# Kernel tuning notes

Measured on AMD Instinct MI355X. Metric: run time of the kernel, lower is better.

## Reference

```python
import jax, jax.numpy as jnp
import numpy as np

H = 16
D_MODEL = 1024
D_K = D_MODEL // H
MAX_REL = 16
REL_VOCAB = 2 * MAX_REL + 1


def _rel_pos_ids(seq_len):
    r = jnp.arange(seq_len)
    dist = r[None, :] - r[:, None]                      # [S,S]
    return jnp.clip(dist, -MAX_REL, MAX_REL) + MAX_REL  # in [0, 2*MAX_REL]


def setup_inputs() -> dict:
    key = jax.random.key(0)
    ks = jax.random.split(key, 16)
    B, S = 2, 2048
    f32 = jnp.float32
    inp = {
        "query": jax.random.normal(ks[0], (B, S, D_MODEL), f32),
        "key": jax.random.normal(ks[1], (B, S, D_MODEL), f32),
        "value": jax.random.normal(ks[2], (B, S, D_MODEL), f32),
        # four nn.Linear(d_model, d_model): W [out,in], b [out]
        "Wq": jax.random.normal(ks[3], (D_MODEL, D_MODEL), f32) * 0.02,
        "bq": jnp.zeros((D_MODEL,), f32),
        "Wk": jax.random.normal(ks[4], (D_MODEL, D_MODEL), f32) * 0.02,
        "bk": jnp.zeros((D_MODEL,), f32),
        "Wv": jax.random.normal(ks[5], (D_MODEL, D_MODEL), f32) * 0.02,
        "bv": jnp.zeros((D_MODEL,), f32),
        "Wo": jax.random.normal(ks[6], (D_MODEL, D_MODEL), f32) * 0.02,
        "bo": jnp.zeros((D_MODEL,), f32),
        # relative-position embedding tables (keys and values)
        "rel_k_table": jax.random.normal(ks[7], (REL_VOCAB, D_K), f32) * 0.02,
        "rel_v_table": jax.random.normal(ks[8], (REL_VOCAB, D_K), f32) * 0.02,
    }
    return inp


def reference(query, key, value, Wq, bq, Wk, bk, Wv, bv, Wo, bo,
              rel_k_table, rel_v_table):
    B, S, E = query.shape
    ids = _rel_pos_ids(S)                    # [S,S] int
    rel_k = rel_k_table[ids]                 # [S,S,d_k]
    rel_v = rel_v_table[ids]                 # [S,S,d_k]

    def proj(x, W, b):
        y = x @ W.T + b                      # [B,S,E]
        return y.reshape(B, S, H, D_K).transpose(0, 2, 1, 3)  # [B,H,S,d_k]

    q = proj(query, Wq, bq)
    k = proj(key, Wk, bk)
    v = proj(value, Wv, bv)

    # NOTE: original has no 1/sqrt(d_k) scaling and ignores mask — faithful.
    logits = jnp.einsum('bhqd,bhkd->bhqk', q, k) \
           + jnp.einsum('bhqd,qkd->bhqk', q, rel_k)
    w = jax.nn.softmax(logits, axis=-1)      # [B,H,S,S]

    x = jnp.einsum('bhqk,bhkd->bhqd', w, v) \
      + jnp.einsum('bhqk,qkd->bhqd', w, rel_v)

    x = x.transpose(0, 2, 1, 3).reshape(B, S, H * D_K)
    return x @ Wo.T + bo
```

## Files before the change

kernel.cpp:

```cpp
#include <hip/hip_runtime.h>
#include <hip/hip_bf16.h>

typedef unsigned short u16;
typedef __attribute__((ext_vector_type(8))) short short8;
typedef __attribute__((ext_vector_type(4))) short short4_t;
typedef __attribute__((ext_vector_type(4))) float f32x4;

#define MFMA16(a, b, c) __builtin_amdgcn_mfma_f32_16x16x32_bf16((a), (b), (c), 0, 0, 0)

#if __has_builtin(__builtin_amdgcn_mfma_f32_16x16x16bf16_1k)
#define MFMAK16(a, b, c) __builtin_amdgcn_mfma_f32_16x16x16bf16_1k((a), (b), (c), 0, 0, 0)
#elif __has_builtin(__builtin_amdgcn_mfma_f32_16x16x16_bf16)
#define MFMAK16(a, b, c) __builtin_amdgcn_mfma_f32_16x16x16_bf16((a), (b), (c), 0, 0, 0)
#else
__device__ __forceinline__ f32x4 mfmak16_asm(short4_t a, short4_t b, f32x4 c) {
  asm("v_mfma_f32_16x16x16_bf16 %0, %1, %2, %0" : "+v"(c) : "v"(a), "v"(b));
  return c;
}
#define MFMAK16(a, b, c) mfmak16_asm((a), (b), (c))
#endif

#define GLOAD_LDS16(gp, lp)                                          \
  __builtin_amdgcn_global_load_lds(                                  \
      (const __attribute__((address_space(1))) void*)(gp),           \
      (__attribute__((address_space(3))) void*)(lp), 16, 0, 0)
#define SBAR() asm volatile("s_barrier" ::: "memory")
#define WAIT_LGKM0() asm volatile("s_waitcnt lgkmcnt(0)" ::: "memory")
#define WAIT_VM0() asm volatile("s_waitcnt vmcnt(0)" ::: "memory")

#define LOG2E 1.44269504088896340736f

__device__ __forceinline__ float us2f(u16 u) {
  union { unsigned int i; float f; } c; c.i = ((unsigned int)u) << 16; return c.f;
}
__device__ __forceinline__ u16 f2us(float f) {
  union { float f; unsigned int i; } c; c.f = f;
  return (u16)((c.i + 0x7fffu + ((c.i >> 16) & 1u)) >> 16);
}
__device__ __forceinline__ unsigned int f2us2(float a, float b) {
  union { __hip_bfloat162 h; unsigned int u; } c;
  c.h = __float22bfloat162_rn(float2{a, b});
  return c.u;
}
__device__ __forceinline__ float exp2fast(float x) {
#if __has_builtin(__builtin_amdgcn_exp2f)
  return __builtin_amdgcn_exp2f(x);
#else
  return exp2f(x);
#endif
}

__global__ __launch_bounds__(256) void cvt_all_kernel(
    const float* x0, const float* x1, const float* x2, const float* w0,
    const float* w1, const float* w2, const float* w3, const float* relk,
    u16* y0, u16* y1, u16* y2, u16* z0, u16* z1, u16* z2, u16* z3,
    u16* relkb) {
  const int z = blockIdx.z;
  if (z == 7) {
    const int i = (blockIdx.x * 256 + threadIdx.x) * 8;
    if (i < 4096) {
      if (i < 2112) {
        const float4 a = *(const float4*)(relk + i);
        const float4 b = *(const float4*)(relk + i + 4);
        unsigned int o[4];
        o[0] = f2us2(a.x, a.y); o[1] = f2us2(a.z, a.w);
        o[2] = f2us2(b.x, b.y); o[3] = f2us2(b.z, b.w);
        *(uint4*)(relkb + i) = *(uint4*)o;
      } else {
        uint4 zz = {0u, 0u, 0u, 0u};
        *(uint4*)(relkb + i) = zz;
      }
    }
    return;
  }
  const float* src; u16* dst; int n;
  switch (z) {
    case 0: src = x0; dst = y0; n = 4194304; break;
    case 1: src = x1; dst = y1; n = 4194304; break;
    case 2: src = x2; dst = y2; n = 4194304; break;
    case 3: src = w0; dst = z0; n = 1048576; break;
    case 4: src = w1; dst = z1; n = 1048576; break;
    case 5: src = w2; dst = z2; n = 1048576; break;
    default: src = w3; dst = z3; n = 1048576; break;
  }
  const int i = (blockIdx.x * 256 + threadIdx.x) * 8;
  if (i < n) {
    const float4 a = *(const float4*)(src + i);
    const float4 b = *(const float4*)(src + i + 4);
    unsigned int o[4];
    o[0] = f2us2(a.x, a.y); o[1] = f2us2(a.z, a.w);
    o[2] = f2us2(b.x, b.y); o[3] = f2us2(b.z, b.w);
    *(uint4*)(dst + i) = *(uint4*)o;
  }
}

template <int MODE, typename OUT, int BM, int BN, int BK>
__device__ __forceinline__ void gemm_body(u16* __restrict__ SM,
                                          const u16* __restrict__ X,
                                          const u16* __restrict__ W,
                                          const float* __restrict__ bias,
                                          OUT* __restrict__ Y, int row0, int col0,
                                          float oscale) {
  constexpr int TM = BM / 32, TN = BN / 32;
  constexpr int CH = BK / 8;
  constexpr int RPG = 64 / CH;
  constexpr int NGA = BM / (4 * RPG);
  constexpr int NGB = BN / (4 * RPG);
  u16* As = SM;
  u16* Bs = SM + BM * BK;
  const int tid = threadIdx.x;
  const int lane = tid & 63;
  const int wid = tid >> 6;
  const int wm = wid >> 1, wn = wid & 1;
  const int l15 = lane & 15, l16 = lane >> 4;
  const int lrow = lane / CH;
  const int lch = lane % CH;

  f32x4 acc[TM][TN];
#pragma unroll
  for (int i = 0; i < TM; i++)
#pragma unroll
    for (int j = 0; j < TN; j++) acc[i][j] = (f32x4){0.f, 0.f, 0.f, 0.f};

  for (int k0 = 0; k0 < 1024; k0 += BK) {
#pragma unroll
    for (int i = 0; i < NGA; i++) {
      const int rb = (wid * NGA + i) * RPG;
      const int row = rb + lrow;
      GLOAD_LDS16(X + (size_t)(row0 + row) * 1024 + k0 + ((lch ^ (row & 7)) * 8),
                  &As[rb * BK]);
    }
#pragma unroll
    for (int i = 0; i < NGB; i++) {
      const int rb = (wid * NGB + i) * RPG;
      const int row = rb + lrow;
      GLOAD_LDS16(W + (size_t)(col0 + row) * 1024 + k0 + ((lch ^ (row & 7)) * 8),
                  &Bs[rb * BK]);
    }
    __syncthreads();
#pragma unroll
    for (int kk = 0; kk < BK / 32; kk++) {
      const int ch = kk * 4 + l16;
      short8 af[TM], bfr[TN];
#pragma unroll
      for (int t = 0; t < TM; t++) {
        const int m = wm * (BM / 2) + t * 16 + l15;
        af[t] = *(const short8*)&As[m * BK + ((ch ^ (m & 7)) * 8)];
      }
#pragma unroll
      for (int t = 0; t < TN; t++) {
        const int n = wn * (BN / 2) + t * 16 + l15;
        bfr[t] = *(const short8*)&Bs[n * BK + ((ch ^ (n & 7)) * 8)];
      }
#pragma unroll
      for (int tm = 0; tm < TM; tm++)
#pragma unroll
        for (int tn = 0; tn < TN; tn++)
          acc[tm][tn] = MFMA16(af[tm], bfr[tn], acc[tm][tn]);
    }
    __syncthreads();
  }

  if (MODE == 0) {
#pragma unroll
    for (int tn = 0; tn < TN; tn++) {
      const int col = col0 + wn * (BN / 2) + tn * 16 + l15;
      const float bv = bias[col];
#pragma unroll
      for (int tm = 0; tm < TM; tm++) {
        const int rowb = row0 + wm * (BM / 2) + tm * 16 + l16 * 4;
#pragma unroll
        for (int r = 0; r < 4; r++)
          Y[(size_t)(rowb + r) * 1024 + col] = (OUT)(acc[tm][tn][r] + bv);
      }
    }
  } else {
    u16* T = SM;
    const int bb = row0 >> 11;
    const int sbase = row0 & 2047;
#pragma unroll
    for (int pass = 0; pass < 2; pass++) {
      __syncthreads();
      if (wm == pass) {
#pragma unroll
        for (int tn = 0; tn < TN; tn++) {
          const int coll = wn * 64 + tn * 16 + l15;
          const float bv = bias[col0 + coll];
#pragma unroll
          for (int tm = 0; tm < TM; tm++) {
            if (MODE == 1) {
#pragma unroll
              for (int r = 0; r < 4; r++)
                T[(tm * 16 + l16 * 4 + r) * 136 + coll] = f2us((acc[tm][tn][r] + bv) * oscale);
            } else {
              unsigned int o[2];
              o[0] = f2us2(acc[tm][tn][0] + bv, acc[tm][tn][1] + bv);
              o[1] = f2us2(acc[tm][tn][2] + bv, acc[tm][tn][3] + bv);
              *(short4_t*)&T[coll * 72 + tm * 16 + l16 * 4] = *(short4_t*)o;
            }
          }
        }
      }
      __syncthreads();
      if (MODE == 1) {
#pragma unroll
        for (int i = 0; i < 8; i++) {
          const int idx = tid + i * 256;
          const int srow = idx >> 5, c4 = idx & 31;
          const short4_t v = *(const short4_t*)&T[srow * 136 + c4 * 4];
          const int col = col0 + c4 * 4;
          const int hh = col >> 6, dd = col & 63;
          const int s = sbase + pass * 64 + srow;
          *(short4_t*)&((u16*)Y)[(((size_t)(bb * 16 + hh)) * 2048 + s) * 64 + dd] = v;
        }
      } else {
#pragma unroll
        for (int i = 0; i < 4; i++) {
          const int idx = tid + i * 256;
          const int cl = idx >> 3, sc = idx & 7;
          const short8 v = *(const short8*)&T[cl * 72 + sc * 8];
          const int col = col0 + cl;
          const int hh = col >> 6, dd = col & 63;
          const int s = sbase + pass * 64 + sc * 8;
          *(short8*)&((u16*)Y)[(((size_t)(bb * 16 + hh)) * 64 + dd) * 2048 + s] = v;
        }
      }
    }
  }
}

__global__ __launch_bounds__(256) void qkv_kernel(
    const u16* Xq, const u16* Xk, const u16* Xv, const u16* Wq, const u16* Wk,
    const u16* Wv, const float* bq, const float* bk, const float* bv, u16* Yq,
    u16* Yk, u16* Yv) {
  __shared__ __align__(16) u16 SM[16384];
  const int z = blockIdx.z;
  const u16* X = z == 0 ? Xq : (z == 1 ? Xk : Xv);
  const u16* W = z == 0 ? Wq : (z == 1 ? Wk : Wv);
  const float* bi = z == 0 ? bq : (z == 1 ? bk : bv);
  u16* Y = z == 0 ? Yq : (z == 1 ? Yk : Yv);
  if (z == 2)
    gemm_body<2, u16, 128, 128, 64>(SM, X, W, bi, Y, blockIdx.x * 128,
                                    blockIdx.y * 128, 1.0f);
  else
    gemm_body<1, u16, 128, 128, 64>(SM, X, W, bi, Y, blockIdx.x * 128,
                                    blockIdx.y * 128,
                                    z == 0 ? LOG2E : 1.0f);
}

__global__ __launch_bounds__(256) void oproj_kernel(const u16* Xc, const u16* Wo,
                                                    const float* bo, float* out) {
  __shared__ __align__(16) u16 SM[16384];
  gemm_body<0, float, 64, 64, 128>(SM, Xc, Wo, bo, out, blockIdx.x * 64,
                                   blockIdx.y * 64, 1.0f);
}

__global__ __launch_bounds__(256, 6) void attn_kernel(
    const u16* __restrict__ Qg, const u16* __restrict__ Kg,
    const u16* __restrict__ Vtg, const u16* __restrict__ relkb,
    const float* __restrict__ relv, u16* __restrict__ ctx) {
  __shared__ __align__(16) u16 KV[8192];
  __shared__ __align__(16) u16 qrelJ[64 * 33];
  __shared__ __align__(16) u16 wsum[64 * 32];

  const int tid = threadIdx.x, lane = tid & 63, wid = tid >> 6;
  const int l15 = lane & 15, l16 = lane >> 4;
  const int bh = blockIdx.x;
  const int b = bh >> 4, h = bh & 15;
  const int by = blockIdx.y;
  const int q0 = by * 64;
  const u16* Qb = Qg + (size_t)bh * 2048 * 64;
  const u16* Kb = Kg + (size_t)bh * 2048 * 64;
  const u16* Vtb = Vtg + (size_t)bh * 64 * 2048;

  const int lrow = lane >> 3;
  const int lchunk = (lane & 7) ^ lrow;
  const int qw = wid * 16;
  const int kq4 = l16 * 4;
  const int qrow = qw + l15;

#pragma unroll
  for (int i = 0; i < 2; i++) {
    const int rb = qw + i * 8;
    GLOAD_LDS16(Qb + (size_t)(q0 + rb + lrow) * 64 + lchunk * 8, &KV[rb * 64]);
  }
  for (int idx = tid; idx < 1024; idx += 256) ((unsigned int*)wsum)[idx] = 0u;
  __syncthreads();

  short8 aq[2];
  {
    const int m = qw + l15;
    aq[0] = *(const short8*)&KV[m * 64 + ((l16 ^ (m & 7)) * 8)];
    aq[1] = *(const short8*)&KV[m * 64 + (((4 + l16) ^ (m & 7)) * 8)];
  }
  {
    f32x4 qa[3];
#pragma unroll
    for (int nt = 0; nt < 3; nt++) {
      qa[nt] = (f32x4){0.f, 0.f, 0.f, 0.f};
#pragma unroll
      for (int kk = 0; kk < 2; kk++) {
        const short8 bf =
            *(const short8*)(relkb + (nt * 16 + l15) * 64 + kk * 32 + l16 * 8);
        qa[nt] = MFMA16(aq[kk], bf, qa[nt]);
      }
    }
#pragma unroll
    for (int nt = 0; nt < 3; nt++) {
      if (nt < 2 || l15 == 0) {
#pragma unroll
        for (int r = 0; r < 4; r++)
          qrelJ[(qw + kq4 + r) * 33 + nt * 16 + l15] = f2us(qa[nt][r]);
      }
    }
  }
  WAIT_LGKM0();
  const float q0r = us2f(qrelJ[qrow * 33 + 0]);
  const float q32r = us2f(qrelJ[qrow * 33 + 32]);
  const f32x4 ebl = (f32x4){q0r, q0r, q0r, q0r};
  const f32x4 ebr = (f32x4){q32r, q32r, q32r, q32r};
  const f32x4 zf = (f32x4){0.f, 0.f, 0.f, 0.f};
  const short4_t ones4 = (short4_t){(short)0x3F80, (short)0x3F80,
                                    (short)0x3F80, (short)0x3F80};

  float wl_p = 0.f, wr_p = 0.f;
  f32x4 SL = zf, SR = zf, SD = zf;
  f32x4 Oacc[4];
#pragma unroll
  for (int t = 0; t < 4; t++) Oacc[t] = zf;

  auto stage = [&](int k0c) {
    SBAR();
#pragma unroll
    for (int i = 0; i < 2; i++) {
      const int rb = qw + i * 8;
      GLOAD_LDS16(Kb + (size_t)(k0c + rb + lrow) * 64 + lchunk * 8, &KV[rb * 64]);
    }
#pragma unroll
    for (int i = 0; i < 2; i++) {
      const int rb = qw + i * 8;
      GLOAD_LDS16(Vtb + (size_t)(rb + lrow) * 2048 + k0c + lchunk * 8,
                  &KV[4096 + rb * 64]);
    }
    WAIT_VM0();
    SBAR();
  };

  auto qk = [&](int tn, f32x4 cin) -> f32x4 {
    const int n = tn * 16 + l15;
    const short8 bk0 = *(const short8*)&KV[n * 64 + ((l16 ^ (n & 7)) * 8)];
    const short8 bk1 = *(const short8*)&KV[n * 64 + (((4 + l16) ^ (n & 7)) * 8)];
    f32x4 s = MFMA16(bk0, aq[0], cin);
    s = MFMA16(bk1, aq[1], s);
    return s;
  };

  auto pvstep = [&](const short4_t* pf) {
    __builtin_amdgcn_s_setprio(1);
#pragma unroll
    for (int td = 0; td < 4; td++) {
      const int row = td * 16 + l15;
      const int rs = row & 7;
#pragma unroll
      for (int kk = 0; kk < 4; kk++) {
        const short4_t vf = *(const short4_t*)&KV[4096 + row * 64 +
                                                  (((kk * 2 + (l16 >> 1)) ^ rs) * 8) +
                                                  (l16 & 1) * 4];
        Oacc[td] = MFMAK16(vf, pf[kk], Oacc[td]);
      }
    }
    __builtin_amdgcn_s_setprio(0);
  };

  auto psum = [&](const short4_t* pf, f32x4& S) {
#pragma unroll
    for (int kk = 0; kk < 4; kk++) S = MFMAK16(ones4, pf[kk], S);
  };

  auto offdiag = [&](f32x4 ebv, f32x4& S) {
    short4_t pf[4];
#pragma unroll
    for (int tn = 0; tn < 4; tn++) {
      const f32x4 sac = qk(tn, ebv);
      union { unsigned int u[2]; short4_t s; } c;
      c.u[0] = f2us2(exp2fast(sac[0]), exp2fast(sac[1]));
      c.u[1] = f2us2(exp2fast(sac[2]), exp2fast(sac[3]));
      pf[tn] = c.s;
    }
    pvstep(pf);
    psum(pf, S);
  };

  auto diag = [&](int k0) {
    short4_t pf[4];
#pragma unroll
    for (int tn = 0; tn < 4; tn++) {
      const f32x4 sac = qk(tn, zf);
      float pv4[4];
#pragma unroll
      for (int r = 0; r < 4; r++) {
        const int kg = k0 + tn * 16 + kq4 + r;
        const int dlt = kg - (q0 + qrow);
        const int jj = (dlt < -16 ? -16 : (dlt > 16 ? 16 : dlt)) + 16;
        const float p = exp2fast(sac[r] + us2f(qrelJ[qrow * 33 + jj]));
        pv4[r] = p;
        if (dlt <= -16) wl_p += p;
        else if (dlt >= 16) wr_p += p;
        else wsum[qrow * 32 + (dlt + 15)] = f2us(p);
      }
      union { unsigned int u[2]; short4_t s; } c;
      c.u[0] = f2us2(pv4[0], pv4[1]);
      c.u[1] = f2us2(pv4[2], pv4[3]);
      pf[tn] = c.s;
    }
    pvstep(pf);
    psum(pf, SD);
  };

  const int dlo = (by >= 1) ? by - 1 : 0;
  const int dhi = (by + 2 <= 32) ? by + 2 : 32;
  for (int kt = 0; kt < dlo; ++kt) { stage(kt * 64); offdiag(ebl, SL); }
  for (int kt = dlo; kt < dhi; ++kt) { stage(kt * 64); diag(kt * 64); }
  for (int kt = dhi; kt < 32; ++kt) { stage(kt * 64); offdiag(ebr, SR); }

  wl_p += __shfl_xor(wl_p, 16); wl_p += __shfl_xor(wl_p, 32);
  wr_p += __shfl_xor(wr_p, 16); wr_p += __shfl_xor(wr_p, 32);
  const float l_total = SL[0] + SR[0] + SD[0];
  const float linv = 1.f / l_total;
  const float wl = (SL[0] + wl_p) * linv;
  const float wr = (SR[0] + wr_p) * linv;

  {
    short4_t relf[4][2];
#pragma unroll
    for (int td = 0; td < 4; td++)
#pragma unroll
      for (int kk = 0; kk < 2; kk++) {
        const int jb = kk * 16 + l16 * 4 + 1;
        const int d = td * 16 + l15;
        union { unsigned int u[2]; short4_t s; } c;
        c.u[0] = f2us2(relv[(jb + 0) * 64 + d], relv[(jb + 1) * 64 + d]);
        c.u[1] = f2us2(relv[(jb + 2) * 64 + d], relv[(jb + 3) * 64 + d]);
        relf[td][kk] = c.s;
      }
    WAIT_LGKM0();
    short4_t wfrag[2];
#pragma unroll
    for (int kk = 0; kk < 2; kk++)
      wfrag[kk] = *(const short4_t*)&wsum[qrow * 32 + kk * 16 + l16 * 4];
#pragma unroll
    for (int td = 0; td < 4; td++)
#pragma unroll
      for (int kk = 0; kk < 2; kk++)
        Oacc[td] = MFMAK16(relf[td][kk], wfrag[kk], Oacc[td]);
  }

#pragma unroll
  for (int td = 0; td < 4; td++) {
    const f32x4 rv0 = *(const f32x4*)&relv[td * 16 + kq4];
    const f32x4 rv32 = *(const f32x4*)&relv[32 * 64 + td * 16 + kq4];
#pragma unroll
    for (int r = 0; r < 4; r++)
      Oacc[td][r] = Oacc[td][r] * linv + wl * rv0[r] + wr * rv32[r];
  }

  SBAR();
#pragma unroll
  for (int td = 0; td < 4; td++) {
    unsigned int o[2];
    o[0] = f2us2(Oacc[td][0], Oacc[td][1]);
    o[1] = f2us2(Oacc[td][2], Oacc[td][3]);
    *(short4_t*)&KV[qrow * 72 + td * 16 + kq4] = *(short4_t*)o;
  }
  WAIT_LGKM0();
  SBAR();
#pragma unroll
  for (int i = 0; i < 2; i++) {
    const int idx = tid + i * 256;
    const int q = idx >> 3, sc = idx & 7;
    const short8 v = *(const short8*)&KV[q * 72 + sc * 8];
    *(short8*)&ctx[((size_t)b * 2048 + q0 + q) * 1024 + h * 64 + sc * 8] = v;
  }
}

extern "C" void kernel_launch(void* const* d_in, const int* in_sizes, int n_in,
                              void* d_out, int out_size, void* d_ws, size_t ws_size,
                              hipStream_t stream) {
  u16* qb = (u16*)d_ws;
  u16* kb = qb + 4194304;
  u16* vtb = kb + 4194304;
  u16* ctx = vtb + 4194304;
  u16* Xq = ctx + 4194304;
  u16* Xk = Xq + 4194304;
  u16* Xv = Xk + 4194304;
  u16* Wqb = Xv + 4194304;
  u16* Wkb = Wqb + 1048576;
  u16* Wvb = Wkb + 1048576;
  u16* Wob = Wvb + 1048576;
  u16* relkb = Wob + 1048576;

  const float* bq = (const float*)d_in[4];
  const float* bk = (const float*)d_in[6];
  const float* bv = (const float*)d_in[8];
  const float* bo = (const float*)d_in[10];
  const float* relk = (const float*)d_in[11];
  const float* relv = (const float*)d_in[12];

  dim3 blk(256);
  cvt_all_kernel<<<dim3(2048, 1, 8), blk, 0, stream>>>(
      (const float*)d_in[0], (const float*)d_in[1], (const float*)d_in[2],
      (const float*)d_in[3], (const float*)d_in[5], (const float*)d_in[7],
      (const float*)d_in[9], relk, Xq, Xk, Xv, Wqb, Wkb, Wvb, Wob, relkb);
  qkv_kernel<<<dim3(32, 8, 3), blk, 0, stream>>>(Xq, Xk, Xv, Wqb, Wkb, Wvb, bq,
                                                 bk, bv, qb, kb, vtb);
  attn_kernel<<<dim3(32, 32), blk, 0, stream>>>(qb, kb, vtb, relkb, relv, ctx);
  oproj_kernel<<<dim3(64, 16), blk, 0, stream>>>(ctx, Wob, bo, (float*)d_out);
}
```

Before: 243.4 us.

## Process 128 query rows per attention block to share K/V tiles across eight waves

The attention kernel now runs 512 threads per block covering 128 query rows, so each staged 64-key K/V tile is loaded once and reused by twice as many waves. This halves global K/V traffic per query and the number of blocks. Diagonal versus off-diagonal handling is now decided per wave at runtime rather than through split loop ranges, and output is written in two passes through shared memory. It risks lower occupancy, larger barrier groups and branch overhead in the main loop.

```diff
diff --git a/kernel.cpp b/kernel.cpp
--- a/kernel.cpp
+++ b/kernel.cpp
@@ -255,41 +255,43 @@
                                    blockIdx.y * 64, 1.0f);
 }
 
-__global__ __launch_bounds__(256, 6) void attn_kernel(
+__global__ __launch_bounds__(512, 4) void attn_kernel(
     const u16* __restrict__ Qg, const u16* __restrict__ Kg,
     const u16* __restrict__ Vtg, const u16* __restrict__ relkb,
     const float* __restrict__ relv, u16* __restrict__ ctx) {
   __shared__ __align__(16) u16 KV[8192];
-  __shared__ __align__(16) u16 qrelJ[64 * 33];
-  __shared__ __align__(16) u16 wsum[64 * 32];
+  __shared__ __align__(16) u16 qrelJ[128 * 33];
+  __shared__ __align__(16) u16 wsum[128 * 32];
 
   const int tid = threadIdx.x, lane = tid & 63, wid = tid >> 6;
   const int l15 = lane & 15, l16 = lane >> 4;
   const int bh = blockIdx.x;
   const int b = bh >> 4, h = bh & 15;
   const int by = blockIdx.y;
-  const int q0 = by * 64;
+  const int q0b = by * 128;
+  const int qt = wid >> 2;
+  const int q0w = q0b + qt * 64;
   const u16* Qb = Qg + (size_t)bh * 2048 * 64;
   const u16* Kb = Kg + (size_t)bh * 2048 * 64;
   const u16* Vtb = Vtg + (size_t)bh * 64 * 2048;
 
   const int lrow = lane >> 3;
   const int lchunk = (lane & 7) ^ lrow;
-  const int qw = wid * 16;
+  const int qw16 = wid * 16;
   const int kq4 = l16 * 4;
-  const int qrow = qw + l15;
+  const int qrow = qw16 + l15;
 
 #pragma unroll
   for (int i = 0; i < 2; i++) {
-    const int rb = qw + i * 8;
-    GLOAD_LDS16(Qb + (size_t)(q0 + rb + lrow) * 64 + lchunk * 8, &KV[rb * 64]);
-  }
-  for (int idx = tid; idx < 1024; idx += 256) ((unsigned int*)wsum)[idx] = 0u;
+    const int rb = qw16 + i * 8;
+    GLOAD_LDS16(Qb + (size_t)(q0b + rb + lrow) * 64 + lchunk * 8, &KV[rb * 64]);
+  }
+  for (int idx = tid; idx < 2048; idx += 512) ((unsigned int*)wsum)[idx] = 0u;
   __syncthreads();
 
   short8 aq[2];
   {
-    const int m = qw + l15;
+    const int m = qrow;
     aq[0] = *(const short8*)&KV[m * 64 + ((l16 ^ (m & 7)) * 8)];
     aq[1] = *(const short8*)&KV[m * 64 + (((4 + l16) ^ (m & 7)) * 8)];
   }
@@ -310,7 +312,7 @@
       if (nt < 2 || l15 == 0) {
 #pragma unroll
         for (int r = 0; r < 4; r++)
-          qrelJ[(qw + kq4 + r) * 33 + nt * 16 + l15] = f2us(qa[nt][r]);
+          qrelJ[(qw16 + kq4 + r) * 33 + nt * 16 + l15] = f2us(qa[nt][r]);
       }
     }
   }
@@ -331,14 +333,9 @@
 
   auto stage = [&](int k0c) {
     SBAR();
-#pragma unroll
-    for (int i = 0; i < 2; i++) {
-      const int rb = qw + i * 8;
+    {
+      const int rb = wid * 8;
       GLOAD_LDS16(Kb + (size_t)(k0c + rb + lrow) * 64 + lchunk * 8, &KV[rb * 64]);
-    }
-#pragma unroll
-    for (int i = 0; i < 2; i++) {
-      const int rb = qw + i * 8;
       GLOAD_LDS16(Vtb + (size_t)(rb + lrow) * 2048 + k0c + lchunk * 8,
                   &KV[4096 + rb * 64]);
     }
@@ -400,7 +397,7 @@
 #pragma unroll
       for (int r = 0; r < 4; r++) {
         const int kg = k0 + tn * 16 + kq4 + r;
-        const int dlt = kg - (q0 + qrow);
+        const int dlt = kg - (q0b + qrow);
         const int jj = (dlt < -16 ? -16 : (dlt > 16 ? 16 : dlt)) + 16;
         const float p = exp2fast(sac[r] + us2f(qrelJ[qrow * 33 + jj]));
         pv4[r] = p;
@@ -417,11 +414,17 @@
     psum(pf, SD);
   };
 
-  const int dlo = (by >= 1) ? by - 1 : 0;
-  const int dhi = (by + 2 <= 32) ? by + 2 : 32;
-  for (int kt = 0; kt < dlo; ++kt) { stage(kt * 64); offdiag(ebl, SL); }
-  for (int kt = dlo; kt < dhi; ++kt) { stage(kt * 64); diag(kt * 64); }
-  for (int kt = dhi; kt < 32; ++kt) { stage(kt * 64); offdiag(ebr, SR); }
+  for (int kt = 0; kt < 32; ++kt) {
+    const int k0 = kt * 64;
+    stage(k0);
+    if (k0 + 79 <= q0w) {
+      offdiag(ebl, SL);
+    } else if (k0 >= q0w + 79) {
+      offdiag(ebr, SR);
+    } else {
+      diag(k0);
+    }
+  }
 
   wl_p += __shfl_xor(wl_p, 16); wl_p += __shfl_xor(wl_p, 32);
   wr_p += __shfl_xor(wr_p, 16); wr_p += __shfl_xor(wr_p, 32);
@@ -466,20 +469,26 @@
 
   SBAR();
 #pragma unroll
-  for (int td = 0; td < 4; td++) {
-    unsigned int o[2];
-    o[0] = f2us2(Oacc[td][0], Oacc[td][1]);
-    o[1] = f2us2(Oacc[td][2], Oacc[td][3]);
-    *(short4_t*)&KV[qrow * 72 + td * 16 + kq4] = *(short4_t*)o;
-  }
-  WAIT_LGKM0();
-  SBAR();
-#pragma unroll
-  for (int i = 0; i < 2; i++) {
-    const int idx = tid + i * 256;
-    const int q = idx >> 3, sc = idx & 7;
-    const short8 v = *(const short8*)&KV[q * 72 + sc * 8];
-    *(short8*)&ctx[((size_t)b * 2048 + q0 + q) * 1024 + h * 64 + sc * 8] = v;
+  for (int pass = 0; pass < 2; pass++) {
+    if (qt == pass) {
+      const int orow = (wid & 3) * 16 + l15;
+#pragma unroll
+      for (int td = 0; td < 4; td++) {
+        unsigned int o[2];
+        o[0] = f2us2(Oacc[td][0], Oacc[td][1]);
+        o[1] = f2us2(Oacc[td][2], Oacc[td][3]);
+        *(short4_t*)&KV[orow * 72 + td * 16 + kq4] = *(short4_t*)o;
+      }
+      WAIT_LGKM0();
+    }
+    SBAR();
+    {
+      const int q = tid >> 3, sc = tid & 7;
+      const short8 v = *(const short8*)&KV[q * 72 + sc * 8];
+      *(short8*)&ctx[((size_t)b * 2048 + q0b + pass * 64 + q) * 1024 + h * 64 +
+                     sc * 8] = v;
+    }
+    SBAR();
   }
 }
 
@@ -513,6 +522,7 @@
       (const float*)d_in[9], relk, Xq, Xk, Xv, Wqb, Wkb, Wvb, Wob, relkb);
   qkv_kernel<<<dim3(32, 8, 3), blk, 0, stream>>>(Xq, Xk, Xv, Wqb, Wkb, Wvb, bq,
                                                  bk, bv, qb, kb, vtb);
-  attn_kernel<<<dim3(32, 32), blk, 0, stream>>>(qb, kb, vtb, relkb, relv, ctx);
+  attn_kernel<<<dim3(32, 16), dim3(512), 0, stream>>>(qb, kb, vtb, relkb, relv,
+                                                      ctx);
   oproj_kernel<<<dim3(64, 16), blk, 0, stream>>>(ctx, Wob, bo, (float*)d_out);
 }
```

Result: no change. 240.3 us (-1.3%).
